# Kernel tuning notes

Hardware: AMD Instinct MI355X
Metric: run time of the kernel (lower is better)

## Reference

```python
import jax, jax.numpy as jnp
import numpy as np

BS, TLEN, NNODE, DIM = 32, 6, 4, 1500
HID = 128; D2 = 2 * HID
LSTMH, LSTMO, KCONV = 64, 128, 3
CONV_OUT = 191
DECAY = 0.7
WIN, STRIDES = (2, 2), (1, 2)
FEAT_IN = LSTMO * CONV_OUT  # 24448


def _bn(x, p, axis):
    # eval-mode BatchNorm: p = [gamma, beta, running_mean, running_var] stacked [4, C]
    sh = [1] * x.ndim; sh[axis] = -1
    g, b, m, v = (p[i].reshape(sh) for i in range(4))
    return (x - m) * (g * jax.lax.rsqrt(v + 1e-5)) + b


def _conv1d(x, w, pad):  # x [B,C,L], w [O,I,K]
    return jax.lax.conv_general_dilated(x, w, (1,), [(pad, pad)],
                                        dimension_numbers=('NCH', 'OIH', 'NCH'))


def _maxpool2(x):  # MaxPool1d(kernel=2, stride=2, padding=1) with -inf padding
    x = jnp.pad(x, ((0, 0), (0, 0), (1, 1)), constant_values=-jnp.inf)
    return jax.lax.reduce_window(x, -jnp.inf, jax.lax.max, (1, 1, 2), (1, 1, 2), 'VALID')


def _mpnn_block(x, w, s, gw, gb, bnA, tw, tb, bnM):
    # x: [bs, tlen, ns, d]; Conv_GraphST windowing + dot-graph + masked adj + 1-hop MPNN + mean pool
    bs, tlen, ns, d = x.shape
    nw = (tlen - w) // s + 1
    con = jnp.stack([x[:, j * s:j * s + w] for j in range(nw)], axis=1)  # [bs,nw,w,ns,d]
    Xc = con.reshape(bs * nw, w * ns, d)  # node index = t*ns + sensor (time-major)
    f = Xc @ gw + gb
    N = w * ns
    eye = jnp.eye(N, dtype=x.dtype)
    Adj = jnp.einsum('bnd,bmd->bnm', f, f)
    Adj = jax.nn.softmax(jax.nn.leaky_relu(Adj - eye * 1e8), axis=-1) + eye
    t = jnp.arange(N) // ns
    mask = DECAY ** jnp.abs(t[:, None] - t[None, :]).astype(x.dtype)  # Mask_Matrix decay
    Adj = Adj * mask
    Xb = _bn(Xc, bnA, -1)  # BN over feature channel (transpose-BN-transpose in torch)
    h = jnp.einsum('bnm,bmd->bnd', Adj, Xb) @ tw + tb
    h = jax.nn.leaky_relu(_bn(h, bnM, -1))
    return h.reshape(bs, nw, w, ns, -1).mean(axis=2)  # mean pool over window-time


def _pos_encoding(tlen, d):
    pos = jnp.arange(tlen, dtype=jnp.float32)[:, None]
    div = jnp.exp(jnp.arange(0, d, 2, dtype=jnp.float32) * (-np.log(100.0) / d))
    pe = jnp.zeros((tlen, d), jnp.float32)
    return pe.at[:, 0::2].set(jnp.sin(pos * div)).at[:, 1::2].set(jnp.cos(pos * div))


def reference(X, conv1_w, bn1, conv2_w, bn2, conv3_w, bn3,
              map2_w, map2_b, bn_map2,
              g1_w, g1_b, bnA1, th1_w, th1_b, bnM1,
              g2_w, g2_b, bnA2, th2_w, th2_b, bnM2,
              fc1_w, fc1_b, fc2_w, fc2_b, fc3_w, fc3_b, fc4_w, fc4_b):
    X = X.reshape(BS, TLEN, NNODE, -1)
    B = BS * TLEN * NNODE
    a = jnp.transpose(X.reshape(B, -1, 1), (0, 2, 1))  # [B,1,L]
    a = _maxpool2(jax.nn.relu(_bn(_conv1d(a, conv1_w, KCONV // 2), bn1, 1)))
    a = _maxpool2(jax.nn.relu(_bn(_conv1d(a, conv2_w, 2), bn2, 1)))
    a = _maxpool2(jax.nn.relu(_bn(_conv1d(a, conv3_w, 3), bn3, 1)))  # [B,LSTMO,CONV_OUT]
    a = a.reshape(B, -1)
    a = _bn(a @ map2_w + map2_b, bn_map2, -1)
    a = a.reshape(BS, TLEN, NNODE, D2)
    a = a + _pos_encoding(TLEN, D2)[None, :, None, :]  # PE over time, per (batch, node)
    out1 = _mpnn_block(a, WIN[0], STRIDES[0], g1_w, g1_b, bnA1, th1_w, th1_b, bnM1)  # [32,5,4,128]
    out2 = _mpnn_block(a, WIN[1], STRIDES[1], g2_w, g2_b, bnA2, th2_w, th2_b, bnM2)  # [32,3,4,128]
    feats = jnp.concatenate([out1.reshape(BS, -1), out2.reshape(BS, -1)], axis=-1)  # [32,4096]
    h = jax.nn.relu(feats @ fc1_w + fc1_b)
    h = jax.nn.relu(h @ fc2_w + fc2_b)
    h = jax.nn.relu(h @ fc3_w + fc3_b)
    return h @ fc4_w + fc4_b


def setup_inputs():
    key = jax.random.key(0)
    ks = iter(jax.random.split(key, 80))
    def rn(shape, scale=1.0):
        return scale * jax.random.normal(next(ks), shape, jnp.float32)
    def bn(c):
        return jnp.stack([1.0 + 0.1 * rn((c,)), 0.1 * rn((c,)), 0.1 * rn((c,)),
                          1.0 + 0.5 * jax.random.uniform(next(ks), (c,), jnp.float32)])
    def lin(i, o):
        return rn((i, o), 1.0 / np.sqrt(i))
    return {
        'X': rn((BS, TLEN, NNODE, DIM)),
        'conv1_w': rn((LSTMH, 1, KCONV), 0.3),
        'bn1': bn(LSTMH),
        'conv2_w': rn((2 * LSTMH, LSTMH, KCONV), 1.0 / np.sqrt(LSTMH * KCONV)),
        'bn2': bn(2 * LSTMH),
        'conv3_w': rn((LSTMO, 2 * LSTMH, KCONV), 1.0 / np.sqrt(2 * LSTMH * KCONV)),
        'bn3': bn(LSTMO),
        'map2_w': lin(FEAT_IN, D2), 'map2_b': rn((D2,), 0.01), 'bn_map2': bn(D2),
        'g1_w': lin(D2, D2), 'g1_b': rn((D2,), 0.01), 'bnA1': bn(D2),
        'th1_w': lin(D2, HID), 'th1_b': rn((HID,), 0.01), 'bnM1': bn(HID),
        'g2_w': lin(D2, D2), 'g2_b': rn((D2,), 0.01), 'bnA2': bn(D2),
        'th2_w': lin(D2, HID), 'th2_b': rn((HID,), 0.01), 'bnM2': bn(HID),
        'fc1_w': lin(4096, D2), 'fc1_b': rn((D2,), 0.01),
        'fc2_w': lin(D2, D2), 'fc2_b': rn((D2,), 0.01),
        'fc3_w': lin(D2, HID), 'fc3_b': rn((HID,), 0.01),
        'fc4_w': lin(HID, 5), 'fc4_b': rn((5,), 0.01),
    }
```

## Files before the change

### kernel.cpp

```cpp
#include <hip/hip_runtime.h>
#include <hip/hip_bf16.h>

#define L1X   1500
#define L1P   751
#define C1    64
#define L2P   377
#define C2    128
#define L3P   191
#define C3    128
#define FEATK 24448
#define D2    256
#define HIDN  128
#define KSTEPS 764

typedef __attribute__((ext_vector_type(8))) short bf16x8;
typedef __attribute__((ext_vector_type(4))) float f32x4;

__device__ __forceinline__ short f2bf(float x) {
    union { float f; unsigned u; } v; v.f = x;
    unsigned r = (v.u + 0x7FFFu + ((v.u >> 16) & 1u)) >> 16;
    return (short)r;
}
__device__ __forceinline__ float bf2f(short s) {
    union { float f; unsigned u; } v; v.u = ((unsigned)(unsigned short)s) << 16;
    return v.f;
}

template<int IC, int KB>
__global__ __launch_bounds__(256)
void k_wprep(const float* __restrict__ w, short* __restrict__ WtHi,
             short* __restrict__ WtLo)
{
    int idx = blockIdx.x * 256 + threadIdx.x;
    if (idx >= 3 * KB * 4 * 128 * 8) return;
    int i    = idx & 7;
    int rest = idx >> 3;
    int c    = rest & 127; rest >>= 7;
    int sub  = rest & 3;   rest >>= 2;
    int kb   = rest % KB;
    int tap  = rest / KB;
    int ic   = kb * 32 + sub * 8 + i;
    float x  = w[(c * IC + ic) * 3 + tap];
    short h  = f2bf(x);
    WtHi[idx] = h;
    WtLo[idx] = f2bf(x - bf2f(h));
}

__global__ __launch_bounds__(256)
void k_wmprep(const float* __restrict__ W, short* __restrict__ Wmhi,
              short* __restrict__ Wmlo)
{
    const int ks  = blockIdx.x >> 2;
    const int sub = blockIdx.x & 3;
    const int n   = threadIdx.x;
    const int kbase = ks * 32 + sub * 8;
    bf16x8 vh, vl;
    #pragma unroll
    for (int i = 0; i < 8; ++i) {
        int k = kbase + i;
        int c = k & 127, ip = k >> 7;
        float x = W[(size_t)(c * 191 + ip) * D2 + n];
        short h = f2bf(x);
        vh[i] = h;
        vl[i] = f2bf(x - bf2f(h));
    }
    size_t off = ((size_t)(ks * 4 + sub) * 256 + n) * 8;
    *(bf16x8*)(Wmhi + off) = vh;
    *(bf16x8*)(Wmlo + off) = vl;
}

__global__ __launch_bounds__(256)
void k_zero(float* __restrict__ p, int n)
{
    int i = blockIdx.x * 256 + threadIdx.x;
    if (i < n) p[i] = 0.f;
}

template<int IC, int KB, int CONVLEN, int POOLLEN, bool HL>
__device__ __forceinline__
void conv_mfma_core(const short* __restrict__ WtHi, const short* __restrict__ WtLo,
                    const short* lhi, const short* llo,
                    const float* sc, const float* bc,
                    float* __restrict__ outp, short* __restrict__ ohi,
                    short* __restrict__ olo, int P0)
{
    const int lane = threadIdx.x & 63;
    const int wave = threadIdx.x >> 6;
    const int l15  = lane & 15;
    const int sub  = lane >> 4;

    f32x4 acc[2][8];
    #pragma unroll
    for (int mf = 0; mf < 2; ++mf)
        #pragma unroll
        for (int nf = 0; nf < 8; ++nf)
            acc[mf][nf] = (f32x4){0.f, 0.f, 0.f, 0.f};

    #pragma unroll
    for (int tap = 0; tap < 3; ++tap) {
        #pragma unroll
        for (int kb = 0; kb < KB; ++kb) {
            bf16x8 ah[2], al[2];
            #pragma unroll
            for (int mf = 0; mf < 2; ++mf) {
                int r = wave * 32 + mf * 16 + l15 + tap;
                int chunk = (kb * 4 + sub) ^ (r & 7);
                int off = r * IC + chunk * 8;
                ah[mf] = *(const bf16x8*)(lhi + off);
                al[mf] = *(const bf16x8*)(llo + off);
            }
            const short* wbh = WtHi + (size_t)(((tap * KB + kb) * 4 + sub) * 128) * 8;
            const short* wbl = WtLo + (size_t)(((tap * KB + kb) * 4 + sub) * 128) * 8;
            #pragma unroll
            for (int nf = 0; nf < 8; ++nf) {
                bf16x8 bh = *(const bf16x8*)(wbh + (nf * 16 + l15) * 8);
                bf16x8 bl = *(const bf16x8*)(wbl + (nf * 16 + l15) * 8);
                #pragma unroll
                for (int mf = 0; mf < 2; ++mf) {
                    acc[mf][nf] = __builtin_amdgcn_mfma_f32_16x16x32_bf16(ah[mf], bh, acc[mf][nf], 0, 0, 0);
                    acc[mf][nf] = __builtin_amdgcn_mfma_f32_16x16x32_bf16(ah[mf], bl, acc[mf][nf], 0, 0, 0);
                    acc[mf][nf] = __builtin_amdgcn_mfma_f32_16x16x32_bf16(al[mf], bh, acc[mf][nf], 0, 0, 0);
                }
            }
        }
    }

    #pragma unroll
    for (int mf = 0; mf < 2; ++mf) {
        int mbase = wave * 32 + mf * 16 + sub * 4;
        #pragma unroll
        for (int nf = 0; nf < 8; ++nf) {
            int c = nf * 16 + l15;
            float s = sc[c], bb = bc[c];
            float v[4];
            #pragma unroll
            for (int rg = 0; rg < 4; ++rg) {
                int p = P0 + mbase + rg;
                float x = fmaxf(acc[mf][nf][rg] * s + bb, 0.f);
                v[rg] = (p >= 0 && p < CONVLEN) ? x : 0.f;
            }
            int i0 = (P0 + mbase + 1) >> 1;
            float u0 = fmaxf(v[0], v[1]);
            float u1 = fmaxf(v[2], v[3]);
            if constexpr (HL) {
                if (i0 < POOLLEN) {
                    short h = f2bf(u0);
                    ohi[(size_t)i0 * 128 + c] = h;
                    olo[(size_t)i0 * 128 + c] = f2bf(u0 - bf2f(h));
                }
                if (i0 + 1 < POOLLEN) {
                    short h = f2bf(u1);
                    ohi[(size_t)(i0 + 1) * 128 + c] = h;
                    olo[(size_t)(i0 + 1) * 128 + c] = f2bf(u1 - bf2f(h));
                }
            } else {
                if (i0 < POOLLEN)     outp[(size_t)i0 * 128 + c] = u0;
                if (i0 + 1 < POOLLEN) outp[(size_t)(i0 + 1) * 128 + c] = u1;
            }
        }
    }
}

__global__ __launch_bounds__(256)
void k_conv2_mfma(const float* __restrict__ X, const float* __restrict__ w1,
                  const float* __restrict__ bn1,
                  const short* __restrict__ Wt2hi, const short* __restrict__ Wt2lo,
                  const float* __restrict__ bn2, float* __restrict__ pool2t,
                  int b_off)
{
    const int blk = blockIdx.x;
    const int bl  = blk / 6, t = blk % 6;
    const int b   = b_off + bl;
    const int P0  = 128 * t - 1;
    const int T0  = 128 * t - 3;
    const int X0  = 256 * t - 8;

    __shared__ __align__(16) float xw[264];
    __shared__ __align__(16) short t1h[130 * 64];
    __shared__ __align__(16) short t1l[130 * 64];
    __shared__ float sb1s[64], sb1b[64], sc2[128], bc2[128];

    const int tid = threadIdx.x;
    for (int g = tid; g < 262; g += 256) {
        int xi = X0 + g;
        xw[g] = (xi >= 0 && xi < L1X) ? X[(size_t)b * L1X + xi] : 0.f;
    }
    if (tid < 64) {
        float s = bn1[tid] * rsqrtf(bn1[192 + tid] + 1e-5f);
        sb1s[tid] = s;
        sb1b[tid] = bn1[64 + tid] - bn1[128 + tid] * s;
    }
    if (tid < 128) {
        float s = bn2[tid] * rsqrtf(bn2[384 + tid] + 1e-5f);
        sc2[tid] = s;
        bc2[tid] = bn2[128 + tid] - bn2[256 + tid] * s;
    }
    __syncthreads();

    for (int idx = tid; idx < 130 * 64; idx += 256) {
        int r = idx >> 6, c = idx & 63;
        int tt = T0 + r;
        float val = 0.f;
        if (tt >= 0 && tt <= 750) {
            float wk0 = w1[c * 3], wk1 = w1[c * 3 + 1], wk2 = w1[c * 3 + 2];
            float s = sb1s[c], bias = sb1b[c];
            float v0 = 0.f, v1 = 0.f;
            int li = 2 * r;
            if (tt >= 1)
                v0 = fmaxf((wk0 * xw[li] + wk1 * xw[li + 1] + wk2 * xw[li + 2]) * s + bias, 0.f);
            if (tt <= 749)
                v1 = fmaxf((wk0 * xw[li + 1] + wk1 * xw[li + 2] + wk2 * xw[li + 3]) * s + bias, 0.f);
            val = fmaxf(v0, v1);
        }
        short h = f2bf(val);
        int chunk = (c >> 3) ^ (r & 7);
        int off = r * 64 + chunk * 8 + (c & 7);
        t1h[off] = h;
        t1l[off] = f2bf(val - bf2f(h));
    }
    __syncthreads();

    conv_mfma_core<64, 2, 753, 377, false>(Wt2hi, Wt2lo, t1h, t1l, sc2, bc2,
                                           pool2t + (size_t)bl * L2P * 128,
                                           nullptr, nullptr, P0);
}

__global__ __launch_bounds__(256)
void k_conv3_mfma(const float* __restrict__ pool2t,
                  const short* __restrict__ Wt3hi, const short* __restrict__ Wt3lo,
                  const float* __restrict__ bn3, short* __restrict__ p3hi,
                  short* __restrict__ p3lo, int b_off)
{
    const int blk = blockIdx.x;
    const int bl  = blk / 3, t = blk % 3;
    const int b   = b_off + bl;
    const int P0  = 128 * t - 1;
    const int I0  = 128 * t - 4;

    __shared__ __align__(16) short t2h[130 * 128];
    __shared__ __align__(16) short t2l[130 * 128];
    __shared__ float sc3[128], bc3[128];

    const int tid = threadIdx.x;
    if (tid < 128) {
        float s = bn3[tid] * rsqrtf(bn3[384 + tid] + 1e-5f);
        sc3[tid] = s;
        bc3[tid] = bn3[128 + tid] - bn3[256 + tid] * s;
    }

    const float* src = pool2t + (size_t)bl * L2P * 128;
    for (int idx = tid; idx < 130 * 32; idx += 256) {
        int r = idx >> 5, q = idx & 31;
        int pr = I0 + r;
        float4 v = make_float4(0.f, 0.f, 0.f, 0.f);
        if (pr >= 0 && pr < L2P) v = *(const float4*)(src + (size_t)pr * 128 + q * 4);
        int chunk = (q >> 1) ^ (r & 7);
        int off = r * 128 + chunk * 8 + (q & 1) * 4;
        *(short4*)(t2h + off) = make_short4(f2bf(v.x), f2bf(v.y), f2bf(v.z), f2bf(v.w));
        short l0 = f2bf(v.x - bf2f(f2bf(v.x)));
        short l1 = f2bf(v.y - bf2f(f2bf(v.y)));
        short l2 = f2bf(v.z - bf2f(f2bf(v.z)));
        short l3 = f2bf(v.w - bf2f(f2bf(v.w)));
        *(short4*)(t2l + off) = make_short4(l0, l1, l2, l3);
    }
    __syncthreads();

    conv_mfma_core<128, 4, 381, 191, true>(Wt3hi, Wt3lo, t2h, t2l, sc3, bc3,
                                           nullptr,
                                           p3hi + (size_t)b * FEATK,
                                           p3lo + (size_t)b * FEATK, P0);
}

__global__ __launch_bounds__(256)
void k_map2_mfma(const short* __restrict__ Ahi, const short* __restrict__ Alo,
                 const short* __restrict__ Wmhi, const short* __restrict__ Wmlo,
                 float* __restrict__ accum)
{
    const int kt   = blockIdx.x & 31;
    const int mt   = blockIdx.x >> 5;
    const int tid  = threadIdx.x;
    const int lane = tid & 63, wave = tid >> 6;
    const int l15  = lane & 15, sub = lane >> 4;
    const int wm   = wave >> 1, wn = wave & 1;
    const int m0   = mt * 64;

    const int s0 = kt * 24;
    const int s1 = (s0 + 24 < KSTEPS) ? s0 + 24 : KSTEPS;

    __shared__ __align__(16) short Ah[2][64 * 40];
    __shared__ __align__(16) short Al[2][64 * 40];

    const int r  = tid >> 2;
    const int kb = tid & 3;
    const size_t abase = (size_t)(m0 + r) * FEATK + kb * 8;
    const int    lbase = r * 40 + kb * 8;

    f32x4 acc[2][8];
    #pragma unroll
    for (int mf = 0; mf < 2; ++mf)
        #pragma unroll
        for (int nf = 0; nf < 8; ++nf)
            acc[mf][nf] = (f32x4){0.f, 0.f, 0.f, 0.f};

    *(bf16x8*)&Ah[0][lbase] = *(const bf16x8*)(Ahi + abase + (size_t)s0 * 32);
    *(bf16x8*)&Al[0][lbase] = *(const bf16x8*)(Alo + abase + (size_t)s0 * 32);

    int cur = 0;
    for (int s = s0; s < s1; ++s) {
        __syncthreads();
        if (s + 1 < s1) {
            *(bf16x8*)&Ah[cur ^ 1][lbase] = *(const bf16x8*)(Ahi + abase + (size_t)(s + 1) * 32);
            *(bf16x8*)&Al[cur ^ 1][lbase] = *(const bf16x8*)(Alo + abase + (size_t)(s + 1) * 32);
        }
        bf16x8 ah[2], al[2];
        #pragma unroll
        for (int mf = 0; mf < 2; ++mf) {
            int off = (wm * 32 + mf * 16 + l15) * 40 + sub * 8;
            ah[mf] = *(const bf16x8*)&Ah[cur][off];
            al[mf] = *(const bf16x8*)&Al[cur][off];
        }
        const short* wb = Wmhi + ((size_t)(s * 4 + sub) * 256 + wn * 128) * 8;
        const short* wl = Wmlo + ((size_t)(s * 4 + sub) * 256 + wn * 128) * 8;
        #pragma unroll
        for (int nf = 0; nf < 8; ++nf) {
            bf16x8 bh = *(const bf16x8*)(wb + (nf * 16 + l15) * 8);
            bf16x8 bl = *(const bf16x8*)(wl + (nf * 16 + l15) * 8);
            #pragma unroll
            for (int mf = 0; mf < 2; ++mf) {
                acc[mf][nf] = __builtin_amdgcn_mfma_f32_16x16x32_bf16(ah[mf], bh, acc[mf][nf], 0, 0, 0);
                acc[mf][nf] = __builtin_amdgcn_mfma_f32_16x16x32_bf16(ah[mf], bl, acc[mf][nf], 0, 0, 0);
                acc[mf][nf] = __builtin_amdgcn_mfma_f32_16x16x32_bf16(al[mf], bh, acc[mf][nf], 0, 0, 0);
            }
        }
        cur ^= 1;
    }

    #pragma unroll
    for (int mf = 0; mf < 2; ++mf) {
        int mrow = m0 + wm * 32 + mf * 16 + sub * 4;
        #pragma unroll
        for (int nf = 0; nf < 8; ++nf) {
            int n = wn * 128 + nf * 16 + l15;
            #pragma unroll
            for (int rg = 0; rg < 4; ++rg)
                atomicAdd(&accum[(size_t)(mrow + rg) * D2 + n], acc[mf][nf][rg]);
        }
    }
}

__global__ __launch_bounds__(256)
void k_map2fin(const float* __restrict__ accum, const float* __restrict__ mb,
               const float* __restrict__ bn, float* __restrict__ out)
{
    const int row = blockIdx.x;
    const int n   = threadIdx.x;
    float acc = accum[(size_t)row * D2 + n];

    float s    = bn[n] * rsqrtf(bn[768 + n] + 1e-5f);
    float beta = bn[256 + n];
    float mu   = bn[512 + n];
    float bias = mb[n];
    int   jj   = n >> 1;
    float freq = expf((float)(2 * jj) * (-4.605170185988092f / 256.f));
    int   t    = (row >> 2) % 6;
    float ang  = (float)t * freq;
    float pe   = (n & 1) ? cosf(ang) : sinf(ang);
    out[(size_t)row * D2 + n] = (acc + bias - mu) * s + beta + pe;
}

__global__ __launch_bounds__(256)
void k_mpnn(const float* __restrict__ a_pe, const float* __restrict__ gw,
            const float* __restrict__ gb, const float* __restrict__ bnA,
            const float* __restrict__ tw, const float* __restrict__ tb_,
            const float* __restrict__ bnM, float* __restrict__ feats,
            int nw, int stride, int base)
{
    const int g  = blockIdx.x;
    const int b  = g / nw, wi = g % nw;
    const int tid = threadIdx.x;

    __shared__ float Xc[8][256];
    __shared__ float Xb[8][256];
    __shared__ float Fs[8][256];
    __shared__ float Adj[8][8];
    __shared__ float hsm[8][128];

    for (int e = tid; e < 2048; e += 256) {
        int nn = e >> 8, d = e & 255;
        int tt = nn >> 2, sn = nn & 3;
        float v = a_pe[(((size_t)(b * 6) + (wi * stride + tt)) * 4 + sn) * D2 + d];
        Xc[nn][d] = v;
        float s = bnA[d] * rsqrtf(bnA[768 + d] + 1e-5f);
        Xb[nn][d] = (v - bnA[512 + d]) * s + bnA[256 + d];
    }
    __syncthreads();

    {
        const int d = tid;
        #pragma unroll
        for (int nn = 0; nn < 8; ++nn) {
            float acc = gb[d];
            for (int k = 0; k < 256; ++k) acc += Xc[nn][k] * gw[(size_t)k * D2 + d];
            Fs[nn][d] = acc;
        }
    }
    __syncthreads();

    if (tid < 64) {
        int nn = tid >> 3, m = tid & 7;
        float s = 0.f;
        for (int d = 0; d < 256; ++d) s += Fs[nn][d] * Fs[m][d];
        if (nn == m) s -= 1e8f;
        s = (s > 0.f) ? s : 0.01f * s;
        Adj[nn][m] = s;
    }
    __syncthreads();

    if (tid < 8) {
        int nn = tid;
        float mx = -1e30f;
        for (int m = 0; m < 8; ++m) mx = fmaxf(mx, Adj[nn][m]);
        float ex[8]; float sum = 0.f;
        for (int m = 0; m < 8; ++m) { ex[m] = expf(Adj[nn][m] - mx); sum += ex[m]; }
        float inv = 1.f / sum;
        for (int m = 0; m < 8; ++m) {
            float v = ex[m] * inv + ((nn == m) ? 1.f : 0.f);
            v *= ((nn >> 2) == (m >> 2)) ? 1.f : 0.7f;
            Adj[nn][m] = v;
        }
    }
    __syncthreads();

    {
        const int d = tid;
        float hm[8];
        #pragma unroll
        for (int nn = 0; nn < 8; ++nn) {
            float a = 0.f;
            #pragma unroll
            for (int m = 0; m < 8; ++m) a += Adj[nn][m] * Xb[m][d];
            hm[nn] = a;
        }
        #pragma unroll
        for (int nn = 0; nn < 8; ++nn) Fs[nn][d] = hm[nn];
    }
    __syncthreads();

    {
        const int o = tid & 127, half = tid >> 7;
        float ms  = bnM[o] * rsqrtf(bnM[384 + o] + 1e-5f);
        float mbe = bnM[128 + o], mmu = bnM[256 + o];
        #pragma unroll
        for (int q = 0; q < 4; ++q) {
            int nn = half + 2 * q;
            float acc = tb_[o];
            for (int d = 0; d < 256; ++d) acc += Fs[nn][d] * tw[(size_t)d * HIDN + o];
            float y = (acc - mmu) * ms + mbe;
            hsm[nn][o] = (y > 0.f) ? y : 0.01f * y;
        }
    }
    __syncthreads();

    for (int e = tid; e < 512; e += 256) {
        int sn = e >> 7, o = e & 127;
        feats[(size_t)b * 4096 + base + (wi * 4 + sn) * HIDN + o] =
            0.5f * (hsm[sn][o] + hsm[4 + sn][o]);
    }
}

__global__ __launch_bounds__(256)
void k_fc1(const float* __restrict__ feats, const float* __restrict__ w1f,
           float* __restrict__ partfc)
{
    const int kc = blockIdx.x >> 3;
    const int nc = blockIdx.x & 7;
    const int tid = threadIdx.x;

    __shared__ float fst[32 * 257];

    for (int idx = tid; idx < 32 * 256; idx += 256) {
        int r = idx >> 8, k = idx & 255;
        fst[r * 257 + k] = feats[(size_t)r * 4096 + kc * 256 + k];
    }
    __syncthreads();

    const int c  = tid & 31;
    const int rg = tid >> 5;
    const float* wp = w1f + (size_t)(kc * 256) * 256 + nc * 32 + c;

    float acc[4] = {0.f, 0.f, 0.f, 0.f};
    for (int k = 0; k < 256; ++k) {
        float wv = wp[(size_t)k * 256];
        #pragma unroll
        for (int j = 0; j < 4; ++j)
            acc[j] += fst[(rg * 4 + j) * 257 + k] * wv;
    }
    #pragma unroll
    for (int j = 0; j < 4; ++j)
        partfc[((size_t)kc * 32 + rg * 4 + j) * 256 + nc * 32 + c] = acc[j];
}

__global__ __launch_bounds__(256)
void k_fc_rest(const float* __restrict__ partfc,
               const float* __restrict__ b1f,
               const float* __restrict__ w2f, const float* __restrict__ b2f,
               const float* __restrict__ w3f, const float* __restrict__ b3f,
               const float* __restrict__ w4f, const float* __restrict__ b4f,
               float* __restrict__ out)
{
    const int b = blockIdx.x;
    const int n = threadIdx.x;
    __shared__ float h1[256], h2[256], h3[128];

    {
        float acc = b1f[n];
        #pragma unroll
        for (int kc = 0; kc < 16; ++kc)
            acc += partfc[((size_t)kc * 32 + b) * 256 + n];
        h1[n] = fmaxf(acc, 0.f);
    }
    __syncthreads();
    {
        float acc = b2f[n];
        for (int k = 0; k < 256; ++k) acc += h1[k] * w2f[(size_t)k * 256 + n];
        h2[n] = fmaxf(acc, 0.f);
    }
    __syncthreads();
    if (n < 128) {
        float acc = b3f[n];
        for (int k = 0; k < 256; ++k) acc += h2[k] * w3f[(size_t)k * 128 + n];
        h3[n] = fmaxf(acc, 0.f);
    }
    __syncthreads();
    if (n < 5) {
        float acc = b4f[n];
        for (int k = 0; k < 128; ++k) acc += h3[k] * w4f[(size_t)k * 5 + n];
        out[b * 5 + n] = acc;
    }
}

extern "C" void kernel_launch(void* const* d_in, const int* in_sizes, int n_in,
                              void* d_out, int out_size, void* d_ws, size_t ws_size,
                              hipStream_t stream)
{
    const float* X      = (const float*)d_in[0];
    const float* w1     = (const float*)d_in[1];
    const float* bn1    = (const float*)d_in[2];
    const float* w2     = (const float*)d_in[3];
    const float* bn2    = (const float*)d_in[4];
    const float* w3     = (const float*)d_in[5];
    const float* bn3    = (const float*)d_in[6];
    const float* map2w  = (const float*)d_in[7];
    const float* map2b  = (const float*)d_in[8];
    const float* bnm2   = (const float*)d_in[9];
    const float* g1w    = (const float*)d_in[10];
    const float* g1b    = (const float*)d_in[11];
    const float* bnA1   = (const float*)d_in[12];
    const float* th1w   = (const float*)d_in[13];
    const float* th1b   = (const float*)d_in[14];
    const float* bnM1   = (const float*)d_in[15];
    const float* g2w    = (const float*)d_in[16];
    const float* g2b    = (const float*)d_in[17];
    const float* bnA2   = (const float*)d_in[18];
    const float* th2w   = (const float*)d_in[19];
    const float* th2b   = (const float*)d_in[20];
    const float* bnM2   = (const float*)d_in[21];
    const float* fc1w   = (const float*)d_in[22];
    const float* fc1b   = (const float*)d_in[23];
    const float* fc2w   = (const float*)d_in[24];
    const float* fc2b   = (const float*)d_in[25];
    const float* fc3w   = (const float*)d_in[26];
    const float* fc3b   = (const float*)d_in[27];
    const float* fc4w   = (const float*)d_in[28];
    const float* fc4b   = (const float*)d_in[29];
    float* out = (float*)d_out;

    float* ws = (float*)d_ws;
    float* pool2t = ws;
    short* p3hi   = (short*)(ws + 4632576);
    short* p3lo   = p3hi + 18776064;
    float* a_pe   = (float*)(p3lo + 18776064);
    float* feats  = a_pe + 196608;
    short* Wt2hi  = (short*)(feats + 131072);
    short* Wt2lo  = Wt2hi + 24576;
    short* Wt3hi  = Wt2lo + 24576;
    short* Wt3lo  = Wt3hi + 49152;
    float* partfc = (float*)(Wt3lo + 49152);
    short* Wmhi   = (short*)(partfc + 131072);
    short* Wmlo   = Wmhi + 6258688;
    float* accum  = ws;

    k_wprep<64, 2><<<96, 256, 0, stream>>>(w2, Wt2hi, Wt2lo);
    k_wprep<128, 4><<<192, 256, 0, stream>>>(w3, Wt3hi, Wt3lo);
    k_wmprep<<<KSTEPS * 4, 256, 0, stream>>>(map2w, Wmhi, Wmlo);

    for (int boff = 0; boff < 768; boff += 96) {
        k_conv2_mfma<<<96 * 6, 256, 0, stream>>>(X, w1, bn1, Wt2hi, Wt2lo, bn2,
                                                 pool2t, boff);
        k_conv3_mfma<<<96 * 3, 256, 0, stream>>>(pool2t, Wt3hi, Wt3lo, bn3,
                                                 p3hi, p3lo, boff);
    }
    k_zero<<<768, 256, 0, stream>>>(accum, 196608);
    k_map2_mfma<<<384, 256, 0, stream>>>(p3hi, p3lo, Wmhi, Wmlo, accum);
    k_map2fin<<<768, 256, 0, stream>>>(accum, map2b, bnm2, a_pe);
    k_mpnn<<<160, 256, 0, stream>>>(a_pe, g1w, g1b, bnA1, th1w, th1b, bnM1,
                                    feats, 5, 1, 0);
    k_mpnn<<<96, 256, 0, stream>>>(a_pe, g2w, g2b, bnA2, th2w, th2b, bnM2,
                                   feats, 3, 2, 2560);
    k_fc1<<<128, 256, 0, stream>>>(feats, fc1w, partfc);
    k_fc_rest<<<32, 256, 0, stream>>>(partfc, fc1b, fc2w, fc2b, fc3w, fc3b,
                                      fc4w, fc4b, out);
}
```

Baseline: 742.8 us.

## Store conv2 output as bf16 hi/lo, enlarge batch chunks, split map2 atomics

```diff
diff --git a/kernel.cpp b/kernel.cpp
--- a/kernel.cpp
+++ b/kernel.cpp
@@ -12,6 +12,7 @@
 #define D2    256
 #define HIDN  128
 #define KSTEPS 764
+#define CHUNK 192
 
 typedef __attribute__((ext_vector_type(8))) short bf16x8;
 typedef __attribute__((ext_vector_type(4))) float f32x4;
@@ -165,8 +166,8 @@
 void k_conv2_mfma(const float* __restrict__ X, const float* __restrict__ w1,
                   const float* __restrict__ bn1,
                   const short* __restrict__ Wt2hi, const short* __restrict__ Wt2lo,
-                  const float* __restrict__ bn2, float* __restrict__ pool2t,
-                  int b_off)
+                  const float* __restrict__ bn2, short* __restrict__ p2hi,
+                  short* __restrict__ p2lo, int b_off)
 {
     const int blk = blockIdx.x;
     const int bl  = blk / 6, t = blk % 6;
@@ -220,13 +221,14 @@
     }
     __syncthreads();
 
-    conv_mfma_core<64, 2, 753, 377, false>(Wt2hi, Wt2lo, t1h, t1l, sc2, bc2,
-                                           pool2t + (size_t)bl * L2P * 128,
-                                           nullptr, nullptr, P0);
-}
-
-__global__ __launch_bounds__(256)
-void k_conv3_mfma(const float* __restrict__ pool2t,
+    conv_mfma_core<64, 2, 753, 377, true>(Wt2hi, Wt2lo, t1h, t1l, sc2, bc2,
+                                          nullptr,
+                                          p2hi + (size_t)bl * L2P * 128,
+                                          p2lo + (size_t)bl * L2P * 128, P0);
+}
+
+__global__ __launch_bounds__(256)
+void k_conv3_mfma(const short* __restrict__ p2hi, const short* __restrict__ p2lo,
                   const short* __restrict__ Wt3hi, const short* __restrict__ Wt3lo,
                   const float* __restrict__ bn3, short* __restrict__ p3hi,
                   short* __restrict__ p3lo, int b_off)
@@ -248,20 +250,20 @@
         bc3[tid] = bn3[128 + tid] - bn3[256 + tid] * s;
     }
 
-    const float* src = pool2t + (size_t)bl * L2P * 128;
+    const short* s2h = p2hi + (size_t)bl * L2P * 128;
+    const short* s2l = p2lo + (size_t)bl * L2P * 128;
     for (int idx = tid; idx < 130 * 32; idx += 256) {
         int r = idx >> 5, q = idx & 31;
         int pr = I0 + r;
-        float4 v = make_float4(0.f, 0.f, 0.f, 0.f);
-        if (pr >= 0 && pr < L2P) v = *(const float4*)(src + (size_t)pr * 128 + q * 4);
+        short4 vh = make_short4(0, 0, 0, 0), vl = make_short4(0, 0, 0, 0);
+        if (pr >= 0 && pr < L2P) {
+            vh = *(const short4*)(s2h + (size_t)pr * 128 + q * 4);
+            vl = *(const short4*)(s2l + (size_t)pr * 128 + q * 4);
+        }
         int chunk = (q >> 1) ^ (r & 7);
         int off = r * 128 + chunk * 8 + (q & 1) * 4;
-        *(short4*)(t2h + off) = make_short4(f2bf(v.x), f2bf(v.y), f2bf(v.z), f2bf(v.w));
-        short l0 = f2bf(v.x - bf2f(f2bf(v.x)));
-        short l1 = f2bf(v.y - bf2f(f2bf(v.y)));
-        short l2 = f2bf(v.z - bf2f(f2bf(v.z)));
-        short l3 = f2bf(v.w - bf2f(f2bf(v.w)));
-        *(short4*)(t2l + off) = make_short4(l0, l1, l2, l3);
+        *(short4*)(t2h + off) = vh;
+        *(short4*)(t2l + off) = vl;
     }
     __syncthreads();
 
@@ -276,16 +278,16 @@
                  const short* __restrict__ Wmhi, const short* __restrict__ Wmlo,
                  float* __restrict__ accum)
 {
-    const int kt   = blockIdx.x & 31;
-    const int mt   = blockIdx.x >> 5;
+    const int kt   = blockIdx.x % 48;
+    const int mt   = blockIdx.x / 48;
     const int tid  = threadIdx.x;
     const int lane = tid & 63, wave = tid >> 6;
     const int l15  = lane & 15, sub = lane >> 4;
     const int wm   = wave >> 1, wn = wave & 1;
     const int m0   = mt * 64;
 
-    const int s0 = kt * 24;
-    const int s1 = (s0 + 24 < KSTEPS) ? s0 + 24 : KSTEPS;
+    const int s0 = kt * 16;
+    const int s1 = (s0 + 16 < KSTEPS) ? s0 + 16 : KSTEPS;
 
     __shared__ __align__(16) short Ah[2][64 * 40];
     __shared__ __align__(16) short Al[2][64 * 40];
@@ -335,6 +337,7 @@
         cur ^= 1;
     }
 
+    float* acct = accum + (size_t)(kt & 7) * 196608;
     #pragma unroll
     for (int mf = 0; mf < 2; ++mf) {
         int mrow = m0 + wm * 32 + mf * 16 + sub * 4;
@@ -343,7 +346,7 @@
             int n = wn * 128 + nf * 16 + l15;
             #pragma unroll
             for (int rg = 0; rg < 4; ++rg)
-                atomicAdd(&accum[(size_t)(mrow + rg) * D2 + n], acc[mf][nf][rg]);
+                atomicAdd(&acct[(size_t)(mrow + rg) * D2 + n], acc[mf][nf][rg]);
         }
     }
 }
@@ -354,7 +357,10 @@
 {
     const int row = blockIdx.x;
     const int n   = threadIdx.x;
-    float acc = accum[(size_t)row * D2 + n];
+    float acc = 0.f;
+    #pragma unroll
+    for (int c = 0; c < 8; ++c)
+        acc += accum[(size_t)c * 196608 + (size_t)row * D2 + n];
 
     float s    = bn[n] * rsqrtf(bn[768 + n] + 1e-5f);
     float beta = bn[256 + n];
@@ -576,8 +582,14 @@
     float* out = (float*)d_out;
 
     float* ws = (float*)d_ws;
-    float* pool2t = ws;
-    short* p3hi   = (short*)(ws + 4632576);
+    const size_t SZ_P2 = (size_t)CHUNK * L2P * 128;
+    short* p2hi  = (short*)ws;
+    short* p2lo  = p2hi + SZ_P2;
+    short* Wmhi  = (short*)ws;
+    short* Wmlo  = Wmhi + 6258688;
+    float* accum = (float*)(Wmlo + 6258688);
+    float* after  = ws + 9264384;
+    short* p3hi   = (short*)after;
     short* p3lo   = p3hi + 18776064;
     float* a_pe   = (float*)(p3lo + 18776064);
     float* feats  = a_pe + 196608;
@@ -586,22 +598,19 @@
     short* Wt3hi  = Wt2lo + 24576;
     short* Wt3lo  = Wt3hi + 49152;
     float* partfc = (float*)(Wt3lo + 49152);
-    short* Wmhi   = (short*)(partfc + 131072);
-    short* Wmlo   = Wmhi + 6258688;
-    float* accum  = ws;
 
     k_wprep<64, 2><<<96, 256, 0, stream>>>(w2, Wt2hi, Wt2lo);
     k_wprep<128, 4><<<192, 256, 0, stream>>>(w3, Wt3hi, Wt3lo);
+
+    for (int boff = 0; boff < 768; boff += CHUNK) {
+        k_conv2_mfma<<<CHUNK * 6, 256, 0, stream>>>(X, w1, bn1, Wt2hi, Wt2lo, bn2,
+                                                    p2hi, p2lo, boff);
+        k_conv3_mfma<<<CHUNK * 3, 256, 0, stream>>>(p2hi, p2lo, Wt3hi, Wt3lo, bn3,
+                                                    p3hi, p3lo, boff);
+    }
     k_wmprep<<<KSTEPS * 4, 256, 0, stream>>>(map2w, Wmhi, Wmlo);
-
-    for (int boff = 0; boff < 768; boff += 96) {
-        k_conv2_mfma<<<96 * 6, 256, 0, stream>>>(X, w1, bn1, Wt2hi, Wt2lo, bn2,
-                                                 pool2t, boff);
-        k_conv3_mfma<<<96 * 3, 256, 0, stream>>>(pool2t, Wt3hi, Wt3lo, bn3,
-                                                 p3hi, p3lo, boff);
-    }
-    k_zero<<<768, 256, 0, stream>>>(accum, 196608);
-    k_map2_mfma<<<384, 256, 0, stream>>>(p3hi, p3lo, Wmhi, Wmlo, accum);
+    k_zero<<<(8 * 196608 + 255) / 256, 256, 0, stream>>>(accum, 8 * 196608);
+    k_map2_mfma<<<576, 256, 0, stream>>>(p3hi, p3lo, Wmhi, Wmlo, accum);
     k_map2fin<<<768, 256, 0, stream>>>(accum, map2b, bnm2, a_pe);
     k_mpnn<<<160, 256, 0, stream>>>(a_pe, g1w, g1b, bnA1, th1w, th1b, bnM1,
                                     feats, 5, 1, 0);
```

New measurement: 679.0 us. -8.6%, faster.
